# Optimization experiments

Hardware: AMD Instinct MI355X
Metric: run time of the kernel (lower is better)

## Reference

```python
import jax, jax.numpy as jnp
import numpy as np

MARGIN = 1.0
EPS = 1e-6  # torch F.pairwise_distance default eps, added elementwise to (x - y)
NEG_INF = -1e30
POS_INF = 1e30


def _pairwise_dist_matrix(e):
    # D[i,j] = || e_i - e_j + EPS ||_2, expanded so we never materialize [B,B,D]:
    # ||d + eps||^2 = ||d||^2 + 2*eps*sum(d) + Dfeat*eps^2,  d = e_i - e_j
    sq = jnp.sum(e * e, axis=1)          # [B]
    s = jnp.sum(e, axis=1)               # [B]
    d2 = (sq[:, None] + sq[None, :] - 2.0 * (e @ e.T)
          + 2.0 * EPS * (s[:, None] - s[None, :])
          + e.shape[1] * (EPS * EPS))
    return jnp.sqrt(jnp.maximum(d2, 0.0))  # [B,B]


def _pdist(x, y):
    # F.pairwise_distance(p=2): ||x - y + eps||
    return jnp.sqrt(jnp.sum(jnp.square(x - y + EPS), axis=-1))


def setup_inputs() -> dict:
    B, D = 4096, 128
    key = jax.random.key(0)
    k1, k2, k3, k4 = jax.random.split(key, 4)
    embedding = jax.random.normal(k1, (B, D), dtype=jnp.float32)
    # label space == batch, each label appears exactly once in the batch
    target_idx = jax.random.permutation(k2, B).astype(jnp.int32)
    positive_idxs = jax.random.bernoulli(k3, 0.02, (B, B))  # [B, L] label-space mask
    negative_idxs = jax.random.bernoulli(k4, 0.5, (B, B))
    return {"embedding": embedding, "target_idx": target_idx,
            "positive_idxs": positive_idxs, "negative_idxs": negative_idxs}


def reference(embedding, target_idx, positive_idxs, negative_idxs):
    # Mining happens under no_grad in the original module.
    dm = jax.lax.stop_gradient(_pairwise_dist_matrix(embedding))  # [B,B]
    # batch j is a positive/negative candidate for anchor i iff its label is flagged
    pos_mask = positive_idxs[:, target_idx]  # [B,B] bool
    neg_mask = negative_idxs[:, target_idx]
    pos_idx = jnp.argmax(jnp.where(pos_mask, dm, NEG_INF), axis=1)  # hardest positive
    neg_idx = jnp.argmin(jnp.where(neg_mask, dm, POS_INF), axis=1)  # hardest negative
    valid = jnp.any(pos_mask, axis=1) & jnp.any(neg_mask, axis=1)
    a = embedding
    p = embedding[pos_idx]
    n = embedding[neg_idx]
    ap = _pdist(a, p)
    an = _pdist(a, n)
    pn = _pdist(p, n)
    loss = jax.nn.relu(ap - jnp.minimum(an, pn) + MARGIN)
    w = valid.astype(loss.dtype)
    return jnp.sum(loss * w) / jnp.maximum(jnp.sum(w), 1.0)
```

## Files before the change

kernel.cpp:

```cpp
#include <hip/hip_runtime.h>
#include <stdint.h>

#define BN 4096
#define DD 128
#define EPSF 1e-6f
#define MARGINF 1.0f

typedef unsigned long long ull;
typedef unsigned short ushort;
typedef short short8 __attribute__((ext_vector_type(8)));
typedef float f32x4 __attribute__((ext_vector_type(4)));

__device__ __forceinline__ unsigned int ord_f32(float f) {
    unsigned int u = __float_as_uint(f);
    return (u & 0x80000000u) ? ~u : (u | 0x80000000u);
}
__device__ __forceinline__ ushort bf16_rne(float x) {
    unsigned int u = __float_as_uint(x);
    return (ushort)((u + 0x7FFFu + ((u >> 16) & 1u)) >> 16);
}
__device__ __forceinline__ unsigned int pack8(ull v) {
    v &= 0x0F0F0F0F0F0F0F0FULL;
    v = (v | (v >> 4)) & 0x00FF00FF00FF00FFULL;
    v = (v | (v >> 8)) & 0x0000FFFF0000FFFFULL;
    v = (v | (v >> 16));
    return (unsigned int)v;
}

__global__ void k_prep(const float* __restrict__ e, const int* __restrict__ tidx,
                       float* __restrict__ sq, float* __restrict__ s,
                       int* __restrict__ inv, ull* __restrict__ pk, ull* __restrict__ nk,
                       unsigned int* __restrict__ ehi) {
    int w = threadIdx.x >> 6, lane = threadIdx.x & 63;
    int row = blockIdx.x * 4 + w;
    float2 v = ((const float2*)(e + (size_t)row * DD))[lane];
    ushort hx = bf16_rne(v.x), hy = bf16_rne(v.y);
    ehi[row * 64 + lane] = (unsigned int)hx | ((unsigned int)hy << 16);
    float ss = v.x + v.y;
    float qq = v.x * v.x + v.y * v.y;
    #pragma unroll
    for (int off = 32; off > 0; off >>= 1) {
        ss += __shfl_down(ss, off);
        qq += __shfl_down(qq, off);
    }
    if (lane == 0) {
        sq[row] = qq; s[row] = ss;
        inv[tidx[row]] = row;
        pk[row] = 0ULL; nk[row] = 0ULL;
    }
}

__global__ __launch_bounds__(256, 4)
void k_select(const ushort* __restrict__ ehi,
              const int* __restrict__ pos, const int* __restrict__ neg,
              const float* __restrict__ sq, const float* __restrict__ s,
              const int* __restrict__ inv,
              ull* __restrict__ pkey, ull* __restrict__ nkey) {
    __shared__ __align__(16) char smem[36864];
    __shared__ float rjl[128];
    __shared__ int jvs[128];

    const int tid = threadIdx.x;
    const int lane = tid & 63;
    const int w = tid >> 6, wr = w >> 1, wc = w & 1;
    const int lrow = lane & 15, quad = lane >> 4;
    const int i0 = blockIdx.x * 128, c0 = blockIdx.y * 128;

    if (tid < 128) {
        int j = inv[c0 + tid];
        jvs[tid] = j;
        rjl[tid] = sq[j] - 2.0f * EPSF * s[j];
    }

    unsigned char* nibP = (unsigned char*)smem;
    unsigned char* nibN = (unsigned char*)(smem + 4096);
    {
        const int4* pbase = (const int4*)(pos + (size_t)i0 * BN + c0);
        const int4* nbase = (const int4*)(neg + (size_t)i0 * BN + c0);
        #pragma unroll
        for (int p = 0; p < 16; p++) {
            int flat = p * 256 + tid;
            int r = flat >> 5, q = flat & 31;
            size_t idx = (size_t)r * (BN / 4) + q;
            int4 P = pbase[idx];
            int4 N = nbase[idx];
            unsigned int pm = (unsigned int)(P.x != 0) | ((unsigned int)(P.y != 0) << 1)
                            | ((unsigned int)(P.z != 0) << 2) | ((unsigned int)(P.w != 0) << 3);
            unsigned int nm = (unsigned int)(N.x != 0) | ((unsigned int)(N.y != 0) << 1)
                            | ((unsigned int)(N.z != 0) << 2) | ((unsigned int)(N.w != 0) << 3);
            nibP[r * 32 + q] = (unsigned char)pm;
            nibN[r * 32 + q] = (unsigned char)nm;
        }
    }
    __syncthreads();

    ull pw, nw;
    {
        int off = (tid >> 1) * 32 + (tid & 1) * 16;
        ull lo = *(const ull*)(nibP + off);
        ull hi = *(const ull*)(nibP + off + 8);
        pw = (ull)pack8(lo) | ((ull)pack8(hi) << 32);
        lo = *(const ull*)(nibN + off);
        hi = *(const ull*)(nibN + off + 8);
        nw = (ull)pack8(lo) | ((ull)pack8(hi) << 32);
    }
    __syncthreads();

    ushort* Bst = (ushort*)smem;
    #pragma unroll
    for (int it = 0; it < 8; it++) {
        int slot = it * 256 + tid;
        int r = slot >> 4, seg16 = slot & 15;
        int kc = seg16 >> 3, seg = seg16 & 7;
        int jr = jvs[r];
        int4 v = ((const int4*)ehi)[(size_t)jr * 16 + seg16];
        *(int4*)(Bst + (kc * 128 + r) * 72 + seg * 8) = v;
    }
    __syncthreads();

    f32x4 acc[4][4];
    #pragma unroll
    for (int rt = 0; rt < 4; rt++)
        #pragma unroll
        for (int ct = 0; ct < 4; ct++)
            acc[rt][ct] = (f32x4){0.f, 0.f, 0.f, 0.f};

    size_t abase[4];
    #pragma unroll
    for (int rt = 0; rt < 4; rt++)
        abase[rt] = (size_t)(i0 + wr * 64 + rt * 16 + lrow) * DD + quad * 8;

    #pragma unroll
    for (int ks = 0; ks < 4; ks++) {
        const int kc = ks >> 1, ksl = ks & 1;
        short8 ah[4];
        #pragma unroll
        for (int rt = 0; rt < 4; rt++)
            ah[rt] = *(const short8*)(ehi + abase[rt] + ks * 32);
        #pragma unroll
        for (int ct = 0; ct < 4; ct++) {
            const int bo = (kc * 128 + wc * 64 + ct * 16 + lrow) * 72 + ksl * 32 + quad * 8;
            short8 bh = *(const short8*)(Bst + bo);
            #pragma unroll
            for (int rt = 0; rt < 4; rt++)
                acc[rt][ct] = __builtin_amdgcn_mfma_f32_16x16x32_bf16(ah[rt], bh, acc[rt][ct], 0, 0, 0);
        }
    }

    __syncthreads();
    ull* pbl = (ull*)smem;
    ull* nbl = (ull*)(smem + 2048);
    pbl[tid] = pw;
    nbl[tid] = nw;
    __syncthreads();

    int jcol[4]; float rjc[4];
    #pragma unroll
    for (int ct = 0; ct < 4; ct++) {
        jcol[ct] = jvs[wc * 64 + ct * 16 + lrow];
        rjc[ct] = rjl[wc * 64 + ct * 16 + lrow];
    }
    ull* scrp = (ull*)(smem + 4096);
    ull* scrn = (ull*)(smem + 20480);
    #pragma unroll
    for (int rt = 0; rt < 4; rt++)
        #pragma unroll
        for (int t = 0; t < 4; t++) {
            const int row = wr * 64 + rt * 16 + quad * 4 + t;
            ull pb = pbl[row * 2 + wc] >> lrow;
            ull nb = nbl[row * 2 + wc] >> lrow;
            float bpv = -3.4e38f, bnv = 3.4e38f;
            int bpi = 0x7FFFFFFF, bni = 0x7FFFFFFF;
            #pragma unroll
            for (int ct = 0; ct < 4; ct++) {
                float m = rjc[ct] - 2.0f * acc[rt][ct][t];
                int j = jcol[ct];
                if ((pb >> (ct * 16)) & 1ULL) {
                    if (m > bpv || (m == bpv && j < bpi)) { bpv = m; bpi = j; }
                }
                if ((nb >> (ct * 16)) & 1ULL) {
                    if (m < bnv || (m == bnv && j < bni)) { bnv = m; bni = j; }
                }
            }
            ull kp = (bpi == 0x7FFFFFFF) ? 0ULL
                   : (((ull)ord_f32(bpv) << 32) | (ull)(0xFFFFFFFFu - (unsigned)bpi));
            ull kn = (bni == 0x7FFFFFFF) ? 0ULL
                   : (((ull)(~ord_f32(bnv)) << 32) | (ull)(0xFFFFFFFFu - (unsigned)bni));
            ull op = __shfl_xor(kp, 8); if (op > kp) kp = op;
            ull on = __shfl_xor(kn, 8); if (on > kn) kn = on;
            if (lrow < 8) {
                scrp[(wc * 8 + lrow) * 128 + row] = kp;
                scrn[(wc * 8 + lrow) * 128 + row] = kn;
            }
        }
    __syncthreads();
    if (tid < 128) {
        ull kp = 0ULL, kn = 0ULL;
        #pragma unroll
        for (int k = 0; k < 16; k++) {
            ull v = scrp[k * 128 + tid]; if (v > kp) kp = v;
            v = scrn[k * 128 + tid];     if (v > kn) kn = v;
        }
        if (kp) atomicMax(&pkey[i0 + tid], kp);
        if (kn) atomicMax(&nkey[i0 + tid], kn);
    }
}

__global__ void k_loss(const float* __restrict__ e,
                       const ull* __restrict__ pkey, const ull* __restrict__ nkey,
                       float* __restrict__ partials) {
    int w = threadIdx.x >> 6, lane = threadIdx.x & 63;
    int row = blockIdx.x * 4 + w;
    ull pk = pkey[row], nk = nkey[row];
    float loss = 0.0f, wt = 0.0f;
    if (pk != 0ULL && nk != 0ULL) {
        int pi = (int)(0xFFFFFFFFu - (unsigned)(pk & 0xFFFFFFFFu));
        int ni = (int)(0xFFFFFFFFu - (unsigned)(nk & 0xFFFFFFFFu));
        float2 av = ((const float2*)(e + (size_t)row * DD))[lane];
        float2 pv = ((const float2*)(e + (size_t)pi * DD))[lane];
        float2 nv = ((const float2*)(e + (size_t)ni * DD))[lane];
        float dx, dy;
        dx = av.x - pv.x + EPSF; dy = av.y - pv.y + EPSF;
        float ap2 = dx * dx + dy * dy;
        dx = av.x - nv.x + EPSF; dy = av.y - nv.y + EPSF;
        float an2 = dx * dx + dy * dy;
        dx = pv.x - nv.x + EPSF; dy = pv.y - nv.y + EPSF;
        float pn2 = dx * dx + dy * dy;
        #pragma unroll
        for (int off = 32; off > 0; off >>= 1) {
            ap2 += __shfl_down(ap2, off);
            an2 += __shfl_down(an2, off);
            pn2 += __shfl_down(pn2, off);
        }
        if (lane == 0) {
            float ap = sqrtf(ap2), an = sqrtf(an2), pn = sqrtf(pn2);
            loss = fmaxf(ap - fminf(an, pn) + MARGINF, 0.0f);
            wt = 1.0f;
        }
    }
    __shared__ float sl[4], sw[4];
    if (lane == 0) { sl[w] = loss; sw[w] = wt; }
    __syncthreads();
    if (threadIdx.x == 0) {
        partials[blockIdx.x * 2 + 0] = sl[0] + sl[1] + sl[2] + sl[3];
        partials[blockIdx.x * 2 + 1] = sw[0] + sw[1] + sw[2] + sw[3];
    }
}

__global__ void k_final(const float* __restrict__ partials, float* __restrict__ out) {
    int tid = threadIdx.x;
    float L = 0.0f, W = 0.0f;
    for (int i = 0; i < 4; i++) {
        int idx = tid + i * 256;
        L += partials[idx * 2];
        W += partials[idx * 2 + 1];
    }
    #pragma unroll
    for (int off = 32; off > 0; off >>= 1) {
        L += __shfl_down(L, off);
        W += __shfl_down(W, off);
    }
    __shared__ float sl[4], sw[4];
    int w = tid >> 6, lane = tid & 63;
    if (lane == 0) { sl[w] = L; sw[w] = W; }
    __syncthreads();
    if (tid == 0) {
        float Lt = sl[0] + sl[1] + sl[2] + sl[3];
        float Wt = sw[0] + sw[1] + sw[2] + sw[3];
        out[0] = Lt / fmaxf(Wt, 1.0f);
    }
}

extern "C" void kernel_launch(void* const* d_in, const int* in_sizes, int n_in,
                              void* d_out, int out_size, void* d_ws, size_t ws_size,
                              hipStream_t stream) {
    const float* e    = (const float*)d_in[0];
    const int*   tidx = (const int*)d_in[1];
    const int*   pos  = (const int*)d_in[2];
    const int*   neg  = (const int*)d_in[3];
    float* out = (float*)d_out;

    ull* pkey  = (ull*)d_ws;
    ull* nkey  = pkey + BN;
    float* sq  = (float*)(nkey + BN);
    float* s   = sq + BN;
    int* inv   = (int*)(s + BN);
    float* partials = (float*)(inv + BN);
    unsigned int* ehi = (unsigned int*)(partials + 2048);

    k_prep<<<BN / 4, 256, 0, stream>>>(e, tidx, sq, s, inv, pkey, nkey, ehi);
    dim3 grid(BN / 128, BN / 128);
    k_select<<<grid, 256, 0, stream>>>((const ushort*)ehi, pos, neg,
                                       sq, s, inv, pkey, nkey);
    k_loss<<<BN / 4, 256, 0, stream>>>(e, pkey, nkey, partials);
    k_final<<<1, 256, 0, stream>>>(partials, out);
}
```

Measured before the change: 184.4 us.

## Specialize waves: half compute MFMA tile, half load masks into bitmasks

Doubles the k_select block to 512 threads, with four waves doing the B gather and bf16 MFMA and four waves concurrently streaming the positive/negative mask rows and packing them into 64-bit bitmasks in registers. This removes the nibble staging in shared memory, the pack8 step and a barrier, and aims to overlap mask loading with the matrix compute. In exchange, each loader thread reads a contiguous 256-byte span per row, so per-instruction coalescing changes, and only half the waves issue mask loads. Occupancy and register limits also change with the new launch bounds.

```diff
diff --git a/kernel.cpp b/kernel.cpp
--- a/kernel.cpp
+++ b/kernel.cpp
@@ -18,13 +18,6 @@
 __device__ __forceinline__ ushort bf16_rne(float x) {
     unsigned int u = __float_as_uint(x);
     return (ushort)((u + 0x7FFFu + ((u >> 16) & 1u)) >> 16);
-}
-__device__ __forceinline__ unsigned int pack8(ull v) {
-    v &= 0x0F0F0F0F0F0F0F0FULL;
-    v = (v | (v >> 4)) & 0x00FF00FF00FF00FFULL;
-    v = (v | (v >> 8)) & 0x0000FFFF0000FFFFULL;
-    v = (v | (v >> 16));
-    return (unsigned int)v;
 }
 
 __global__ void k_prep(const float* __restrict__ e, const int* __restrict__ tidx,
@@ -50,15 +43,18 @@
     }
 }
 
-__global__ __launch_bounds__(256, 4)
+__global__ __launch_bounds__(512)
 void k_select(const ushort* __restrict__ ehi,
               const int* __restrict__ pos, const int* __restrict__ neg,
               const float* __restrict__ sq, const float* __restrict__ s,
               const int* __restrict__ inv,
               ull* __restrict__ pkey, ull* __restrict__ nkey) {
     __shared__ __align__(16) char smem[36864];
+    __shared__ ull pbl[256], nbl[256];
     __shared__ float rjl[128];
     __shared__ int jvs[128];
+
+    ushort* Bst = (ushort*)smem;
 
     const int tid = threadIdx.x;
     const int lane = tid & 63;
@@ -71,128 +67,111 @@
         jvs[tid] = j;
         rjl[tid] = sq[j] - 2.0f * EPSF * s[j];
     }
-
-    unsigned char* nibP = (unsigned char*)smem;
-    unsigned char* nibN = (unsigned char*)(smem + 4096);
-    {
-        const int4* pbase = (const int4*)(pos + (size_t)i0 * BN + c0);
-        const int4* nbase = (const int4*)(neg + (size_t)i0 * BN + c0);
-        #pragma unroll
-        for (int p = 0; p < 16; p++) {
-            int flat = p * 256 + tid;
-            int r = flat >> 5, q = flat & 31;
-            size_t idx = (size_t)r * (BN / 4) + q;
-            int4 P = pbase[idx];
-            int4 N = nbase[idx];
+    __syncthreads();
+
+    if (tid < 256) {
+        #pragma unroll
+        for (int it = 0; it < 8; it++) {
+            int slot = it * 256 + tid;
+            int r = slot >> 4, seg16 = slot & 15;
+            int kc = seg16 >> 3, seg = seg16 & 7;
+            int jr = jvs[r];
+            int4 v = ((const int4*)ehi)[(size_t)jr * 16 + seg16];
+            *(int4*)(Bst + (kc * 128 + r) * 72 + seg * 8) = v;
+        }
+    }
+    __syncthreads();
+
+    f32x4 acc[4][4];
+    if (tid < 256) {
+        #pragma unroll
+        for (int rt = 0; rt < 4; rt++)
+            #pragma unroll
+            for (int ct = 0; ct < 4; ct++)
+                acc[rt][ct] = (f32x4){0.f, 0.f, 0.f, 0.f};
+        size_t abase[4];
+        #pragma unroll
+        for (int rt = 0; rt < 4; rt++)
+            abase[rt] = (size_t)(i0 + wr * 64 + rt * 16 + lrow) * DD + quad * 8;
+        #pragma unroll
+        for (int ks = 0; ks < 4; ks++) {
+            const int kc = ks >> 1, ksl = ks & 1;
+            short8 ah[4];
+            #pragma unroll
+            for (int rt = 0; rt < 4; rt++)
+                ah[rt] = *(const short8*)(ehi + abase[rt] + ks * 32);
+            #pragma unroll
+            for (int ct = 0; ct < 4; ct++) {
+                const int bo = (kc * 128 + wc * 64 + ct * 16 + lrow) * 72 + ksl * 32 + quad * 8;
+                short8 bh = *(const short8*)(Bst + bo);
+                #pragma unroll
+                for (int rt = 0; rt < 4; rt++)
+                    acc[rt][ct] = __builtin_amdgcn_mfma_f32_16x16x32_bf16(ah[rt], bh, acc[rt][ct], 0, 0, 0);
+            }
+        }
+    } else {
+        const int t2 = tid - 256;
+        const int r = t2 >> 1, h = t2 & 1;
+        const int4* pr4 = (const int4*)(pos + (size_t)(i0 + r) * BN + c0 + h * 64);
+        const int4* nr4 = (const int4*)(neg + (size_t)(i0 + r) * BN + c0 + h * 64);
+        ull pw = 0ULL, nw = 0ULL;
+        #pragma unroll
+        for (int g = 0; g < 16; g++) {
+            int4 P = pr4[g];
+            int4 N = nr4[g];
             unsigned int pm = (unsigned int)(P.x != 0) | ((unsigned int)(P.y != 0) << 1)
                             | ((unsigned int)(P.z != 0) << 2) | ((unsigned int)(P.w != 0) << 3);
             unsigned int nm = (unsigned int)(N.x != 0) | ((unsigned int)(N.y != 0) << 1)
                             | ((unsigned int)(N.z != 0) << 2) | ((unsigned int)(N.w != 0) << 3);
-            nibP[r * 32 + q] = (unsigned char)pm;
-            nibN[r * 32 + q] = (unsigned char)nm;
-        }
-    }
-    __syncthreads();
-
-    ull pw, nw;
-    {
-        int off = (tid >> 1) * 32 + (tid & 1) * 16;
-        ull lo = *(const ull*)(nibP + off);
-        ull hi = *(const ull*)(nibP + off + 8);
-        pw = (ull)pack8(lo) | ((ull)pack8(hi) << 32);
-        lo = *(const ull*)(nibN + off);
-        hi = *(const ull*)(nibN + off + 8);
-        nw = (ull)pack8(lo) | ((ull)pack8(hi) << 32);
-    }
-    __syncthreads();
-
-    ushort* Bst = (ushort*)smem;
-    #pragma unroll
-    for (int it = 0; it < 8; it++) {
-        int slot = it * 256 + tid;
-        int r = slot >> 4, seg16 = slot & 15;
-        int kc = seg16 >> 3, seg = seg16 & 7;
-        int jr = jvs[r];
-        int4 v = ((const int4*)ehi)[(size_t)jr * 16 + seg16];
-        *(int4*)(Bst + (kc * 128 + r) * 72 + seg * 8) = v;
-    }
-    __syncthreads();
-
-    f32x4 acc[4][4];
-    #pragma unroll
-    for (int rt = 0; rt < 4; rt++)
-        #pragma unroll
-        for (int ct = 0; ct < 4; ct++)
-            acc[rt][ct] = (f32x4){0.f, 0.f, 0.f, 0.f};
-
-    size_t abase[4];
-    #pragma unroll
-    for (int rt = 0; rt < 4; rt++)
-        abase[rt] = (size_t)(i0 + wr * 64 + rt * 16 + lrow) * DD + quad * 8;
-
-    #pragma unroll
-    for (int ks = 0; ks < 4; ks++) {
-        const int kc = ks >> 1, ksl = ks & 1;
-        short8 ah[4];
-        #pragma unroll
-        for (int rt = 0; rt < 4; rt++)
-            ah[rt] = *(const short8*)(ehi + abase[rt] + ks * 32);
-        #pragma unroll
-        for (int ct = 0; ct < 4; ct++) {
-            const int bo = (kc * 128 + wc * 64 + ct * 16 + lrow) * 72 + ksl * 32 + quad * 8;
-            short8 bh = *(const short8*)(Bst + bo);
-            #pragma unroll
-            for (int rt = 0; rt < 4; rt++)
-                acc[rt][ct] = __builtin_amdgcn_mfma_f32_16x16x32_bf16(ah[rt], bh, acc[rt][ct], 0, 0, 0);
-        }
-    }
-
-    __syncthreads();
-    ull* pbl = (ull*)smem;
-    ull* nbl = (ull*)(smem + 2048);
-    pbl[tid] = pw;
-    nbl[tid] = nw;
-    __syncthreads();
-
-    int jcol[4]; float rjc[4];
-    #pragma unroll
-    for (int ct = 0; ct < 4; ct++) {
-        jcol[ct] = jvs[wc * 64 + ct * 16 + lrow];
-        rjc[ct] = rjl[wc * 64 + ct * 16 + lrow];
-    }
+            pw |= ((ull)pm) << (g * 4);
+            nw |= ((ull)nm) << (g * 4);
+        }
+        pbl[t2] = pw;
+        nbl[t2] = nw;
+    }
+    __syncthreads();
+
     ull* scrp = (ull*)(smem + 4096);
     ull* scrn = (ull*)(smem + 20480);
-    #pragma unroll
-    for (int rt = 0; rt < 4; rt++)
-        #pragma unroll
-        for (int t = 0; t < 4; t++) {
-            const int row = wr * 64 + rt * 16 + quad * 4 + t;
-            ull pb = pbl[row * 2 + wc] >> lrow;
-            ull nb = nbl[row * 2 + wc] >> lrow;
-            float bpv = -3.4e38f, bnv = 3.4e38f;
-            int bpi = 0x7FFFFFFF, bni = 0x7FFFFFFF;
-            #pragma unroll
-            for (int ct = 0; ct < 4; ct++) {
-                float m = rjc[ct] - 2.0f * acc[rt][ct][t];
-                int j = jcol[ct];
-                if ((pb >> (ct * 16)) & 1ULL) {
-                    if (m > bpv || (m == bpv && j < bpi)) { bpv = m; bpi = j; }
+    if (tid < 256) {
+        int jcol[4]; float rjc[4];
+        #pragma unroll
+        for (int ct = 0; ct < 4; ct++) {
+            jcol[ct] = jvs[wc * 64 + ct * 16 + lrow];
+            rjc[ct] = rjl[wc * 64 + ct * 16 + lrow];
+        }
+        #pragma unroll
+        for (int rt = 0; rt < 4; rt++)
+            #pragma unroll
+            for (int t = 0; t < 4; t++) {
+                const int row = wr * 64 + rt * 16 + quad * 4 + t;
+                ull pb = pbl[row * 2 + wc] >> lrow;
+                ull nb = nbl[row * 2 + wc] >> lrow;
+                float bpv = -3.4e38f, bnv = 3.4e38f;
+                int bpi = 0x7FFFFFFF, bni = 0x7FFFFFFF;
+                #pragma unroll
+                for (int ct = 0; ct < 4; ct++) {
+                    float m = rjc[ct] - 2.0f * acc[rt][ct][t];
+                    int j = jcol[ct];
+                    if ((pb >> (ct * 16)) & 1ULL) {
+                        if (m > bpv || (m == bpv && j < bpi)) { bpv = m; bpi = j; }
+                    }
+                    if ((nb >> (ct * 16)) & 1ULL) {
+                        if (m < bnv || (m == bnv && j < bni)) { bnv = m; bni = j; }
+                    }
                 }
-                if ((nb >> (ct * 16)) & 1ULL) {
-                    if (m < bnv || (m == bnv && j < bni)) { bnv = m; bni = j; }
+                ull kp = (bpi == 0x7FFFFFFF) ? 0ULL
+                       : (((ull)ord_f32(bpv) << 32) | (ull)(0xFFFFFFFFu - (unsigned)bpi));
+                ull kn = (bni == 0x7FFFFFFF) ? 0ULL
+                       : (((ull)(~ord_f32(bnv)) << 32) | (ull)(0xFFFFFFFFu - (unsigned)bni));
+                ull op = __shfl_xor(kp, 8); if (op > kp) kp = op;
+                ull on = __shfl_xor(kn, 8); if (on > kn) kn = on;
+                if (lrow < 8) {
+                    scrp[(wc * 8 + lrow) * 128 + row] = kp;
+                    scrn[(wc * 8 + lrow) * 128 + row] = kn;
                 }
             }
-            ull kp = (bpi == 0x7FFFFFFF) ? 0ULL
-                   : (((ull)ord_f32(bpv) << 32) | (ull)(0xFFFFFFFFu - (unsigned)bpi));
-            ull kn = (bni == 0x7FFFFFFF) ? 0ULL
-                   : (((ull)(~ord_f32(bnv)) << 32) | (ull)(0xFFFFFFFFu - (unsigned)bni));
-            ull op = __shfl_xor(kp, 8); if (op > kp) kp = op;
-            ull on = __shfl_xor(kn, 8); if (on > kn) kn = on;
-            if (lrow < 8) {
-                scrp[(wc * 8 + lrow) * 128 + row] = kp;
-                scrn[(wc * 8 + lrow) * 128 + row] = kn;
-            }
-        }
+    }
     __syncthreads();
     if (tid < 128) {
         ull kp = 0ULL, kn = 0ULL;
@@ -290,7 +269,7 @@
 
     k_prep<<<BN / 4, 256, 0, stream>>>(e, tidx, sq, s, inv, pkey, nkey, ehi);
     dim3 grid(BN / 128, BN / 128);
-    k_select<<<grid, 256, 0, stream>>>((const ushort*)ehi, pos, neg,
+    k_select<<<grid, 512, 0, stream>>>((const ushort*)ehi, pos, neg,
                                        sq, s, inv, pkey, nkey);
     k_loss<<<BN / 4, 256, 0, stream>>>(e, pkey, nkey, partials);
     k_final<<<1, 256, 0, stream>>>(partials, out);
```

New measurement: 220.5 us. +19.6%, slower.
